# Kernel optimization log

Hardware: AMD Instinct MI355X
Metric: run time of the kernel (lower is better)

## Reference

```python
import jax, jax.numpy as jnp
import numpy as np

B, N, NFEAT = 64, 384, 16
E = 3
NHID, NOUT = 128, 128
ST_HID, ST_OUT = 64, 16


def _xavier(key, shape, fan_in, fan_out):
    a = jnp.sqrt(6.0 / (fan_in + fan_out))
    return jax.random.uniform(key, shape, jnp.float32, -a, a)


def setup_inputs() -> dict:
    key = jax.random.key(0)
    ks = jax.random.split(key, 10)
    x = jax.random.normal(ks[0], (B, N, NFEAT), jnp.float32)
    adj = jax.random.uniform(ks[1], (B, E, N, N), jnp.float32)
    emb_w = _xavier(ks[2], (NFEAT, NFEAT), NFEAT, NFEAT)            # Linear(nfeat,nfeat,bias=False)
    gc1_w = _xavier(ks[3], (E, NFEAT, NHID), NFEAT, NHID)           # (edge_dim,in,out)
    gc2_w = _xavier(ks[4], (E, NHID, NHID), NHID, NHID)             # single middle layer (num_layers-2=1)
    gc3_w = _xavier(ks[5], (E, NHID, NOUT), NHID, NOUT)
    st_w1 = _xavier(ks[6], (ST_HID, NOUT), NOUT, ST_HID)            # nn.Linear stores (out,in)
    st_b1 = jnp.zeros((ST_HID,), jnp.float32)
    st_w2 = jnp.full((2 * ST_OUT, ST_HID), 1e-10, jnp.float32)      # init.constant_(linear2.weight, 1e-10)
    st_b2 = jnp.zeros((2 * ST_OUT,), jnp.float32)
    rescale_w = jnp.zeros((1,), jnp.float32)                        # Rescale weight init zero
    return {"x": x, "adj": adj, "emb_w": emb_w, "gc1_w": gc1_w, "gc2_w": gc2_w,
            "gc3_w": gc3_w, "st_w1": st_w1, "st_b1": st_b1, "st_w2": st_w2,
            "st_b2": st_b2, "rescale_w": rescale_w}


def _rgcn_layer(h, adj, W, relu):
    # support: einsum('bid,edh->beih'), aggregate: einsum('beij,bejh->beih'), then sum over e
    support = jnp.einsum('bnd,edh->benh', h, W)
    out = jnp.einsum('bemn,benh->bemh', adj, support)
    if relu:
        out = jax.nn.relu(out)
    return out.sum(axis=1)  # aggregate='sum' over edge types


def reference(x, adj, emb_w, gc1_w, gc2_w, gc3_w, st_w1, st_b1, st_w2, st_b2, rescale_w):
    h = x @ emb_w.T                                   # emb Linear, no bias
    h = _rgcn_layer(h, adj, gc1_w, True)
    h = _rgcn_layer(h, adj, gc2_w, True)
    h = _rgcn_layer(h, adj, gc3_w, False)             # gc3: use_relu=False
    flat = h.reshape(-1, h.shape[-1])                 # (B*N, nout)
    z = jnp.tanh(flat @ st_w1.T + st_b1) @ st_w2.T + st_b2
    s, t = z[:, :ST_OUT], z[:, ST_OUT:]
    s = jnp.exp(rescale_w) * jnp.tanh(s)              # Rescale(tanh(s))
    return jnp.stack([s, t])                          # (2, B*N, ST_OUT)
```

## Files before the change

kernel.cpp:

```cpp
#include <hip/hip_runtime.h>
#include <math.h>

#define ROWS 24576
#define ADJ_BE (384*384)

typedef _Float16 h4v __attribute__((ext_vector_type(4)));
typedef _Float16 h8v __attribute__((ext_vector_type(8)));
typedef float f32x4 __attribute__((ext_vector_type(4)));

#define SPLIT_SCALE 2048.0f
#define INV_SPLIT_SCALE (1.0f / 2048.0f)

__global__ __launch_bounds__(256) void k_h0split(const float* __restrict__ x,
        const float* __restrict__ emb_w, _Float16* __restrict__ Hh, _Float16* __restrict__ Hl) {
    __shared__ float embL[256];
    int t = threadIdx.x;
    if (t < 64) *(float4*)&embL[4 * t] = *(const float4*)(emb_w + 4 * t);
    __syncthreads();
    int gid = blockIdx.x * 256 + t;
    int b = gid / 384, r = gid % 384;
    const float* xp = x + (size_t)gid * 16;
    float xr[16];
    *(float4*)&xr[0]  = *(const float4*)(xp);
    *(float4*)&xr[4]  = *(const float4*)(xp + 4);
    *(float4*)&xr[8]  = *(const float4*)(xp + 8);
    *(float4*)&xr[12] = *(const float4*)(xp + 12);
    size_t base = (size_t)b * 16 * 384 + r;
#pragma unroll
    for (int d = 0; d < 16; ++d) {
        float acc = 0.f;
#pragma unroll
        for (int k = 0; k < 16; ++k) acc = fmaf(xr[k], embL[d * 16 + k], acc);
        _Float16 h = (_Float16)acc;
        Hh[base + (size_t)d * 384] = h;
        Hl[base + (size_t)d * 384] = (_Float16)((acc - (float)h) * SPLIT_SCALE);
    }
}

__global__ __launch_bounds__(256) void k_adj16(const float* __restrict__ adj,
        const _Float16* __restrict__ Hh, const _Float16* __restrict__ Hl,
        float* __restrict__ T1) {
    int mt = blockIdx.x, e = blockIdx.y, b = blockIdx.z;
    const float* A = adj + (size_t)(b * 3 + e) * ADJ_BE + (size_t)mt * 64 * 384;
    const _Float16* BH = Hh + (size_t)b * 16 * 384;
    const _Float16* BL = Hl + (size_t)b * 16 * 384;

    __shared__ _Float16 Af[2][4][4][17][8];

    int t = threadIdx.x;
    int wave = t >> 6, lane = t & 63;
    int l16 = lane & 15, quad = lane >> 4;
    int r0s = t >> 3, q4s = t & 7;

    f32x4 acc0 = f32x4{0.f, 0.f, 0.f, 0.f};
    f32x4 acc1 = f32x4{0.f, 0.f, 0.f, 0.f};

    float4 ra[2];
    h8v rbh, rbl;
#pragma unroll
    for (int p = 0; p < 2; ++p)
        ra[p] = *(const float4*)(A + (size_t)(r0s + 32 * p) * 384 + 4 * q4s);
    rbh = *(const h8v*)(BH + (size_t)l16 * 384 + 8 * quad);
    rbl = *(const h8v*)(BL + (size_t)l16 * 384 + 8 * quad);

    for (int kc = 0; kc < 12; ++kc) {
#pragma unroll
        for (int p = 0; p < 2; ++p) {
            int r = r0s + 32 * p;
            float vv[4] = {ra[p].x, ra[p].y, ra[p].z, ra[p].w};
            h4v hh, ll;
#pragma unroll
            for (int c = 0; c < 4; ++c) {
                _Float16 h = (_Float16)vv[c];
                hh[c] = h;
                ll[c] = (_Float16)((vv[c] - (float)h) * SPLIT_SCALE);
            }
            *(h4v*)&Af[0][r >> 4][q4s >> 1][r & 15][(q4s & 1) * 4] = hh;
            *(h4v*)&Af[1][r >> 4][q4s >> 1][r & 15][(q4s & 1) * 4] = ll;
        }
        h8v b_h = rbh, b_l = rbl;
        __syncthreads();
        if (kc + 1 < 12) {
            int kn = (kc + 1) * 32;
#pragma unroll
            for (int p = 0; p < 2; ++p)
                ra[p] = *(const float4*)(A + (size_t)(r0s + 32 * p) * 384 + kn + 4 * q4s);
            rbh = *(const h8v*)(BH + (size_t)l16 * 384 + kn + 8 * quad);
            rbl = *(const h8v*)(BL + (size_t)l16 * 384 + kn + 8 * quad);
        }
        h8v a_h = *(const h8v*)&Af[0][wave][quad][l16][0];
        h8v a_l = *(const h8v*)&Af[1][wave][quad][l16][0];
        acc0 = __builtin_amdgcn_mfma_f32_16x16x32_f16(a_h, b_h, acc0, 0, 0, 0);
        acc1 = __builtin_amdgcn_mfma_f32_16x16x32_f16(a_h, b_l, acc1, 0, 0, 0);
        acc1 = __builtin_amdgcn_mfma_f32_16x16x32_f16(a_l, b_h, acc1, 0, 0, 0);
        __syncthreads();
    }
    float* Tp = T1 + ((size_t)(b * 3 + e) * 384 + (size_t)mt * 64 + wave * 16) * 16;
#pragma unroll
    for (int reg = 0; reg < 4; ++reg) {
        float v = fmaf(acc1[reg], INV_SPLIT_SCALE, acc0[reg]);
        Tp[(quad * 4 + reg) * 16 + l16] = v;
    }
}

__global__ __launch_bounds__(256) void k_l1s2(const float* __restrict__ T1,
        const float* __restrict__ W1, float* __restrict__ h1) {
    __shared__ float wL[3][16][128];
    __shared__ float tL[3][64][17];
    int t = threadIdx.x;
    int rt = blockIdx.x;
    int b = rt / 6, m0 = (rt % 6) * 64;
#pragma unroll
    for (int p = 0; p < 6; ++p) {
        int idx = t + p * 256;
        float4 v = *(const float4*)(W1 + (size_t)idx * 4);
        int e = idx / 512, rem = idx % 512;
        int d = rem >> 5, q = rem & 31;
        *(float4*)&wL[e][d][q * 4] = v;
    }
#pragma unroll
    for (int p = 0; p < 3; ++p) {
        int idx = t + p * 256;
        int e = idx >> 8, rem = idx & 255;
        int r = rem >> 2, q = rem & 3;
        float4 v = *(const float4*)(T1 + ((size_t)(b * 3 + e) * 384 + m0 + r) * 16 + q * 4);
        tL[e][r][q*4+0] = v.x; tL[e][r][q*4+1] = v.y; tL[e][r][q*4+2] = v.z; tL[e][r][q*4+3] = v.w;
    }
    __syncthreads();
    int tx = t & 31;
    int ty = t >> 5;
    float tot[8][4] = {};
#pragma unroll
    for (int e = 0; e < 3; ++e) {
        float acc[8][4] = {};
#pragma unroll
        for (int d = 0; d < 16; ++d) {
            float a[8], w[4];
#pragma unroll
            for (int i = 0; i < 8; ++i) a[i] = tL[e][ty + 8 * i][d];
#pragma unroll
            for (int j = 0; j < 4; ++j) w[j] = wL[e][d][tx + 32 * j];
#pragma unroll
            for (int i = 0; i < 8; ++i)
#pragma unroll
                for (int j = 0; j < 4; ++j)
                    acc[i][j] = fmaf(a[i], w[j], acc[i][j]);
        }
#pragma unroll
        for (int i = 0; i < 8; ++i)
#pragma unroll
            for (int j = 0; j < 4; ++j)
                tot[i][j] += fmaxf(acc[i][j], 0.f);
    }
    float* out = h1 + (size_t)rt * 64 * 128;
#pragma unroll
    for (int i = 0; i < 8; ++i)
#pragma unroll
        for (int j = 0; j < 4; ++j)
            out[(ty + 8 * i) * 128 + tx + 32 * j] = tot[i][j];
}

__global__ __launch_bounds__(256) void k_support(const float* __restrict__ hin,
        const float* __restrict__ W, _Float16* __restrict__ Sh, _Float16* __restrict__ Sl) {
    int rt = blockIdx.x, e = blockIdx.y;
    int b = rt / 6, n0 = (rt % 6) * 64;
    const float* Hp = hin + (size_t)rt * 64 * 128;
    const float* Wp = W + (size_t)e * 128 * 128;
    __shared__ float aT[32][68];
    __shared__ float bT[32][132];
    int t = threadIdx.x;
    int tx = t & 15;
    int ty = t >> 4;
    float acc[4][8] = {};
    for (int k0 = 0; k0 < 128; k0 += 32) {
        __syncthreads();
#pragma unroll
        for (int p = 0; p < 2; ++p) {
            int idx = t + p * 256;
            int r = idx >> 3, q = idx & 7;
            float4 v = *(const float4*)(Hp + (size_t)r * 128 + k0 + q * 4);
            aT[q*4+0][r] = v.x; aT[q*4+1][r] = v.y; aT[q*4+2][r] = v.z; aT[q*4+3][r] = v.w;
        }
#pragma unroll
        for (int p = 0; p < 4; ++p) {
            int idx = t + p * 256;
            int r = idx >> 5, q = idx & 31;
            *(float4*)&bT[r][q * 4] = *(const float4*)(Wp + (size_t)(k0 + r) * 128 + q * 4);
        }
        __syncthreads();
#pragma unroll
        for (int k = 0; k < 32; ++k) {
            float4 av = *(const float4*)&aT[k][4 * ty];
            float4 b0 = *(const float4*)&bT[k][4 * tx];
            float4 b1 = *(const float4*)&bT[k][64 + 4 * tx];
            float a[4] = {av.x, av.y, av.z, av.w};
            float bb[8] = {b0.x, b0.y, b0.z, b0.w, b1.x, b1.y, b1.z, b1.w};
#pragma unroll
            for (int i = 0; i < 4; ++i)
#pragma unroll
                for (int j = 0; j < 8; ++j)
                    acc[i][j] = fmaf(a[i], bb[j], acc[i][j]);
        }
    }
    size_t base = (size_t)(b * 3 + e) * 128 * 384;
#pragma unroll
    for (int j = 0; j < 8; ++j) {
        int n = (j < 4) ? (4 * tx + j) : (64 + 4 * tx + j - 4);
        h4v hh, ll;
#pragma unroll
        for (int i = 0; i < 4; ++i) {
            float v = acc[i][j];
            _Float16 h = (_Float16)v;
            hh[i] = h;
            ll[i] = (_Float16)((v - (float)h) * SPLIT_SCALE);
        }
        size_t off = base + (size_t)n * 384 + n0 + 4 * ty;
        *(h4v*)(Sh + off) = hh;
        *(h4v*)(Sl + off) = ll;
    }
}

template <int RELU>
__global__ __launch_bounds__(256, 3) void k_adj_mfma(const float* __restrict__ adj,
        const _Float16* __restrict__ Sh, const _Float16* __restrict__ Sl,
        float* __restrict__ out) {
    int bid = blockIdx.x;
    int xcd = bid & 7, l = bid >> 3;
    int pair = xcd * 24 + (l >> 2);
    int mt = l & 3;
    int b = pair / 3;
    const float* A = adj + (size_t)pair * ADJ_BE + (size_t)mt * 96 * 384;
    const _Float16* Bh = Sh + (size_t)pair * 128 * 384;
    const _Float16* Bl = Sl + (size_t)pair * 128 * 384;
    float* O = out + ((size_t)b * 384 + mt * 96) * 128;

    __shared__ _Float16 Af[2][6][4][17][8];
    __shared__ _Float16 Bf[2][8][4][17][8];

    int t = threadIdx.x;
    int wave = t >> 6, lane = t & 63;
    int l16 = lane & 15, quad = lane >> 4;
    int wm = wave >> 1, wn = wave & 1;
    int r0s = t >> 3, q4s = t & 7;

    f32x4 acc0[3][4], acc1[3][4];
#pragma unroll
    for (int i = 0; i < 3; ++i)
#pragma unroll
        for (int j = 0; j < 4; ++j) {
            acc0[i][j] = f32x4{0.f, 0.f, 0.f, 0.f};
            acc1[i][j] = f32x4{0.f, 0.f, 0.f, 0.f};
        }

    float4 ra[3];
    h8v rb[4];
#pragma unroll
    for (int p = 0; p < 3; ++p)
        ra[p] = *(const float4*)(A + (size_t)(r0s + 32 * p) * 384 + 4 * q4s);
#pragma unroll
    for (int p = 0; p < 4; ++p) {
        int si = t + 256 * (p & 1);
        int n = si >> 2, q8 = si & 3;
        const _Float16* Bsrc = (p < 2) ? Bh : Bl;
        rb[p] = *(const h8v*)(Bsrc + (size_t)n * 384 + 8 * q8);
    }

    for (int k0 = 0; k0 < 384; k0 += 32) {
#pragma unroll
        for (int p = 0; p < 3; ++p) {
            int r = r0s + 32 * p;
            float vv[4] = {ra[p].x, ra[p].y, ra[p].z, ra[p].w};
            h4v hh, ll;
#pragma unroll
            for (int c = 0; c < 4; ++c) {
                _Float16 h = (_Float16)vv[c];
                hh[c] = h;
                ll[c] = (_Float16)((vv[c] - (float)h) * SPLIT_SCALE);
            }
            *(h4v*)&Af[0][r >> 4][q4s >> 1][r & 15][(q4s & 1) * 4] = hh;
            *(h4v*)&Af[1][r >> 4][q4s >> 1][r & 15][(q4s & 1) * 4] = ll;
        }
#pragma unroll
        for (int p = 0; p < 4; ++p) {
            int si = t + 256 * (p & 1);
            int n = si >> 2, q8 = si & 3;
            *(h8v*)&Bf[p >> 1][n >> 4][q8][n & 15][0] = rb[p];
        }
        __syncthreads();
        if (k0 + 32 < 384) {
            int kn = k0 + 32;
#pragma unroll
            for (int p = 0; p < 3; ++p)
                ra[p] = *(const float4*)(A + (size_t)(r0s + 32 * p) * 384 + kn + 4 * q4s);
#pragma unroll
            for (int p = 0; p < 4; ++p) {
                int si = t + 256 * (p & 1);
                int n = si >> 2, q8 = si & 3;
                const _Float16* Bsrc = (p < 2) ? Bh : Bl;
                rb[p] = *(const h8v*)(Bsrc + (size_t)n * 384 + kn + 8 * q8);
            }
        }
        h8v a_h[3], a_l[3];
#pragma unroll
        for (int i = 0; i < 3; ++i) {
            a_h[i] = *(const h8v*)&Af[0][3 * wm + i][quad][l16][0];
            a_l[i] = *(const h8v*)&Af[1][3 * wm + i][quad][l16][0];
        }
#pragma unroll
        for (int j = 0; j < 4; ++j) {
            h8v b_h = *(const h8v*)&Bf[0][4 * wn + j][quad][l16][0];
            h8v b_l = *(const h8v*)&Bf[1][4 * wn + j][quad][l16][0];
#pragma unroll
            for (int i = 0; i < 3; ++i) {
                acc0[i][j] = __builtin_amdgcn_mfma_f32_16x16x32_f16(a_h[i], b_h, acc0[i][j], 0, 0, 0);
                acc1[i][j] = __builtin_amdgcn_mfma_f32_16x16x32_f16(a_h[i], b_l, acc1[i][j], 0, 0, 0);
                acc1[i][j] = __builtin_amdgcn_mfma_f32_16x16x32_f16(a_l[i], b_h, acc1[i][j], 0, 0, 0);
            }
        }
        __syncthreads();
    }
#pragma unroll
    for (int i = 0; i < 3; ++i) {
        int r0 = 48 * wm + 16 * i + quad * 4;
#pragma unroll
        for (int j = 0; j < 4; ++j) {
            int gc = 64 * wn + 16 * j + l16;
#pragma unroll
            for (int reg = 0; reg < 4; ++reg) {
                float v = fmaf(acc1[i][j][reg], INV_SPLIT_SCALE, acc0[i][j][reg]);
                if (RELU) v = fmaxf(v, 0.f);
                atomicAdd(O + (size_t)(r0 + reg) * 128 + gc, v);
            }
        }
    }
}

__global__ void k_zero(float* __restrict__ p, int n4) {
    int i = blockIdx.x * blockDim.x + threadIdx.x;
    if (i < n4) ((float4*)p)[i] = float4{0.f, 0.f, 0.f, 0.f};
}

__global__ __launch_bounds__(256) void k_head(const float* __restrict__ h3,
        const float* __restrict__ st_w1, const float* __restrict__ st_b1,
        const float* __restrict__ st_w2, const float* __restrict__ st_b2,
        const float* __restrict__ rescale_w, float* __restrict__ out) {
    __shared__ float hL[64][132];
    __shared__ float w1L[64][132];
    __shared__ float ytL[64][68];
    __shared__ float w2L[32][68];
    __shared__ float b1L[64], b2L[32];
    int t = threadIdx.x;
    int r0 = blockIdx.x * 64;
#pragma unroll
    for (int p = 0; p < 8; ++p) {
        int idx = t + p * 256;
        int r = idx >> 5, q = idx & 31;
        *(float4*)&hL[r][q * 4] = *(const float4*)(h3 + (size_t)(r0 + r) * 128 + q * 4);
    }
#pragma unroll
    for (int p = 0; p < 8; ++p) {
        int idx = t + p * 256;
        int r = idx >> 5, q = idx & 31;
        *(float4*)&w1L[r][q * 4] = *(const float4*)(st_w1 + (size_t)r * 128 + q * 4);
    }
#pragma unroll
    for (int p = 0; p < 2; ++p) {
        int idx = t + p * 256;
        int r = idx >> 4, q = idx & 15;
        *(float4*)&w2L[r][q * 4] = *(const float4*)(st_w2 + (size_t)r * 64 + q * 4);
    }
    if (t < 64) b1L[t] = st_b1[t];
    else if (t < 96) b2L[t - 64] = st_b2[t - 64];
    __syncthreads();
    int tx = t & 15, ty = t >> 4;
    float acc[4][4] = {};
    for (int d = 0; d < 128; ++d) {
        float a[4], w[4];
#pragma unroll
        for (int i = 0; i < 4; ++i) a[i] = hL[ty + 16 * i][d];
#pragma unroll
        for (int j = 0; j < 4; ++j) w[j] = w1L[tx + 16 * j][d];
#pragma unroll
        for (int i = 0; i < 4; ++i)
#pragma unroll
            for (int j = 0; j < 4; ++j)
                acc[i][j] = fmaf(a[i], w[j], acc[i][j]);
    }
#pragma unroll
    for (int i = 0; i < 4; ++i)
#pragma unroll
        for (int j = 0; j < 4; ++j)
            ytL[ty + 16 * i][tx + 16 * j] = tanhf(acc[i][j] + b1L[tx + 16 * j]);
    __syncthreads();
    int tx8 = t & 7, ty32 = t >> 3;
    float acc2[2][4] = {};
    for (int d = 0; d < 64; ++d) {
        float a[2], w[4];
#pragma unroll
        for (int i = 0; i < 2; ++i) a[i] = ytL[ty32 + 32 * i][d];
#pragma unroll
        for (int j = 0; j < 4; ++j) w[j] = w2L[tx8 + 8 * j][d];
#pragma unroll
        for (int i = 0; i < 2; ++i)
#pragma unroll
            for (int j = 0; j < 4; ++j)
                acc2[i][j] = fmaf(a[i], w[j], acc2[i][j]);
    }
    float er = expf(rescale_w[0]);
#pragma unroll
    for (int i = 0; i < 2; ++i) {
        int r = r0 + ty32 + 32 * i;
#pragma unroll
        for (int j = 0; j < 4; ++j) {
            int c = tx8 + 8 * j;
            float z = acc2[i][j] + b2L[c];
            if (c < 16) out[(size_t)r * 16 + c] = er * tanhf(z);
            else        out[(size_t)(ROWS + r) * 16 + (c - 16)] = z;
        }
    }
}

extern "C" void kernel_launch(void* const* d_in, const int* in_sizes, int n_in,
                              void* d_out, int out_size, void* d_ws, size_t ws_size,
                              hipStream_t stream) {
    const float* x     = (const float*)d_in[0];
    const float* adj   = (const float*)d_in[1];
    const float* emb_w = (const float*)d_in[2];
    const float* gc1   = (const float*)d_in[3];
    const float* gc2   = (const float*)d_in[4];
    const float* gc3   = (const float*)d_in[5];
    const float* st_w1 = (const float*)d_in[6];
    const float* st_b1 = (const float*)d_in[7];
    const float* st_w2 = (const float*)d_in[8];
    const float* st_b2 = (const float*)d_in[9];
    const float* resc  = (const float*)d_in[10];
    float* out = (float*)d_out;
    float* ws  = (float*)d_ws;

    float* T1 = ws;
    float* hA = T1 + 1179648;
    float* hB = hA + 3145728;
    _Float16* Sh = (_Float16*)(hB + 3145728);
    _Float16* Sl = Sh + 9437184;
    _Float16* Hh = (_Float16*)hB;
    _Float16* Hl = Hh + 393216;

    k_h0split<<<96, 256, 0, stream>>>(x, emb_w, Hh, Hl);
    k_adj16<<<dim3(6, 3, 64), 256, 0, stream>>>(adj, Hh, Hl, T1);
    k_l1s2<<<384, 256, 0, stream>>>(T1, gc1, hA);
    k_support<<<dim3(384, 3), 256, 0, stream>>>(hA, gc2, Sh, Sl);
    k_zero<<<3072, 256, 0, stream>>>(hB, 786432);
    k_adj_mfma<1><<<768, 256, 0, stream>>>(adj, Sh, Sl, hB);
    k_support<<<dim3(384, 3), 256, 0, stream>>>(hB, gc3, Sh, Sl);
    k_zero<<<3072, 256, 0, stream>>>(hA, 786432);
    k_adj_mfma<0><<<768, 256, 0, stream>>>(adj, Sh, Sl, hA);
    k_head<<<384, 256, 0, stream>>>(hA, st_w1, st_b1, st_w2, st_b2, resc, out);
}
```

Measured before the change: 434.7 us.

## Fuse edge-type sum into adjacency MFMA kernel, replacing atomics with direct stores

Each block now owns a 48-row tile of one batch and loops over all three edge types in sequence. It applies the ReLU per edge type and accumulates into registers, so it can write its output with plain stores. This removes the zero-fill kernels and the float atomicAdds to global memory. In exchange the grid shrinks from 768 to 512 blocks with smaller per-block M tiles, so each block re-reads the B (support) tiles more per output row. Occupancy is also lowered to 2 blocks per SIMD hint, and half the threads sit idle during A tile loads.

```diff
diff --git a/kernel.cpp b/kernel.cpp
--- a/kernel.cpp
+++ b/kernel.cpp
@@ -221,61 +221,69 @@
 }
 
 template <int RELU>
-__global__ __launch_bounds__(256, 3) void k_adj_mfma(const float* __restrict__ adj,
+__global__ __launch_bounds__(256, 2) void k_adj_fused(const float* __restrict__ adj,
         const _Float16* __restrict__ Sh, const _Float16* __restrict__ Sl,
         float* __restrict__ out) {
     int bid = blockIdx.x;
     int xcd = bid & 7, l = bid >> 3;
-    int pair = xcd * 24 + (l >> 2);
-    int mt = l & 3;
-    int b = pair / 3;
-    const float* A = adj + (size_t)pair * ADJ_BE + (size_t)mt * 96 * 384;
-    const _Float16* Bh = Sh + (size_t)pair * 128 * 384;
-    const _Float16* Bl = Sl + (size_t)pair * 128 * 384;
-    float* O = out + ((size_t)b * 384 + mt * 96) * 128;
-
-    __shared__ _Float16 Af[2][6][4][17][8];
+    int b = xcd * 8 + (l >> 3);
+    int mt = l & 7;
+    const float* A0 = adj + (size_t)(b * 3) * ADJ_BE + (size_t)mt * 48 * 384;
+    const _Float16* Bh0 = Sh + (size_t)(b * 3) * 128 * 384;
+    const _Float16* Bl0 = Sl + (size_t)(b * 3) * 128 * 384;
+    float* O = out + ((size_t)b * 384 + mt * 48) * 128;
+
+    __shared__ _Float16 Af[2][3][4][17][8];
     __shared__ _Float16 Bf[2][8][4][17][8];
 
     int t = threadIdx.x;
     int wave = t >> 6, lane = t & 63;
     int l16 = lane & 15, quad = lane >> 4;
-    int wm = wave >> 1, wn = wave & 1;
     int r0s = t >> 3, q4s = t & 7;
 
-    f32x4 acc0[3][4], acc1[3][4];
+    f32x4 acc0[3][2], acc1[3][2], tot[3][2];
 #pragma unroll
     for (int i = 0; i < 3; ++i)
 #pragma unroll
-        for (int j = 0; j < 4; ++j) {
+        for (int j = 0; j < 2; ++j) {
             acc0[i][j] = f32x4{0.f, 0.f, 0.f, 0.f};
             acc1[i][j] = f32x4{0.f, 0.f, 0.f, 0.f};
-        }
-
-    float4 ra[3];
+            tot[i][j]  = f32x4{0.f, 0.f, 0.f, 0.f};
+        }
+
+    float4 ra[2];
     h8v rb[4];
-#pragma unroll
-    for (int p = 0; p < 3; ++p)
-        ra[p] = *(const float4*)(A + (size_t)(r0s + 32 * p) * 384 + 4 * q4s);
+
+    const float* Ap = A0;
+    const _Float16* Bhp = Bh0;
+    const _Float16* Blp = Bl0;
+    int kn = 0;
+
+#pragma unroll
+    for (int p = 0; p < 2; ++p)
+        if (p == 0 || t < 128)
+            ra[p] = *(const float4*)(Ap + (size_t)(r0s + 32 * p) * 384 + kn + 4 * q4s);
 #pragma unroll
     for (int p = 0; p < 4; ++p) {
         int si = t + 256 * (p & 1);
         int n = si >> 2, q8 = si & 3;
-        const _Float16* Bsrc = (p < 2) ? Bh : Bl;
-        rb[p] = *(const h8v*)(Bsrc + (size_t)n * 384 + 8 * q8);
-    }
-
-    for (int k0 = 0; k0 < 384; k0 += 32) {
-#pragma unroll
-        for (int p = 0; p < 3; ++p) {
+        const _Float16* Bsrc = (p < 2) ? Bhp : Blp;
+        rb[p] = *(const h8v*)(Bsrc + (size_t)n * 384 + kn + 8 * q8);
+    }
+    kn += 32;
+
+    for (int c = 0; c < 36; ++c) {
+#pragma unroll
+        for (int p = 0; p < 2; ++p) {
+            if (p == 1 && t >= 128) break;
             int r = r0s + 32 * p;
             float vv[4] = {ra[p].x, ra[p].y, ra[p].z, ra[p].w};
             h4v hh, ll;
 #pragma unroll
-            for (int c = 0; c < 4; ++c) {
-                _Float16 h = (_Float16)vv[c];
-                hh[c] = h;
-                ll[c] = (_Float16)((vv[c] - (float)h) * SPLIT_SCALE);
+            for (int cc = 0; cc < 4; ++cc) {
+                _Float16 h = (_Float16)vv[cc];
+                hh[cc] = h;
+                ll[cc] = (_Float16)((vv[cc] - (float)h) * SPLIT_SCALE);
             }
             *(h4v*)&Af[0][r >> 4][q4s >> 1][r & 15][(q4s & 1) * 4] = hh;
             *(h4v*)&Af[1][r >> 4][q4s >> 1][r & 15][(q4s & 1) * 4] = ll;
@@ -287,29 +295,36 @@
             *(h8v*)&Bf[p >> 1][n >> 4][q8][n & 15][0] = rb[p];
         }
         __syncthreads();
-        if (k0 + 32 < 384) {
-            int kn = k0 + 32;
-#pragma unroll
-            for (int p = 0; p < 3; ++p)
-                ra[p] = *(const float4*)(A + (size_t)(r0s + 32 * p) * 384 + kn + 4 * q4s);
+        if (c + 1 < 36) {
+            if (kn == 384) {
+                kn = 0;
+                Ap += (size_t)ADJ_BE;
+                Bhp += (size_t)128 * 384;
+                Blp += (size_t)128 * 384;
+            }
+#pragma unroll
+            for (int p = 0; p < 2; ++p)
+                if (p == 0 || t < 128)
+                    ra[p] = *(const float4*)(Ap + (size_t)(r0s + 32 * p) * 384 + kn + 4 * q4s);
 #pragma unroll
             for (int p = 0; p < 4; ++p) {
                 int si = t + 256 * (p & 1);
                 int n = si >> 2, q8 = si & 3;
-                const _Float16* Bsrc = (p < 2) ? Bh : Bl;
+                const _Float16* Bsrc = (p < 2) ? Bhp : Blp;
                 rb[p] = *(const h8v*)(Bsrc + (size_t)n * 384 + kn + 8 * q8);
             }
+            kn += 32;
         }
         h8v a_h[3], a_l[3];
 #pragma unroll
         for (int i = 0; i < 3; ++i) {
-            a_h[i] = *(const h8v*)&Af[0][3 * wm + i][quad][l16][0];
-            a_l[i] = *(const h8v*)&Af[1][3 * wm + i][quad][l16][0];
-        }
-#pragma unroll
-        for (int j = 0; j < 4; ++j) {
-            h8v b_h = *(const h8v*)&Bf[0][4 * wn + j][quad][l16][0];
-            h8v b_l = *(const h8v*)&Bf[1][4 * wn + j][quad][l16][0];
+            a_h[i] = *(const h8v*)&Af[0][i][quad][l16][0];
+            a_l[i] = *(const h8v*)&Af[1][i][quad][l16][0];
+        }
+#pragma unroll
+        for (int j = 0; j < 2; ++j) {
+            h8v b_h = *(const h8v*)&Bf[0][2 * wave + j][quad][l16][0];
+            h8v b_l = *(const h8v*)&Bf[1][2 * wave + j][quad][l16][0];
 #pragma unroll
             for (int i = 0; i < 3; ++i) {
                 acc0[i][j] = __builtin_amdgcn_mfma_f32_16x16x32_f16(a_h[i], b_h, acc0[i][j], 0, 0, 0);
@@ -317,27 +332,34 @@
                 acc1[i][j] = __builtin_amdgcn_mfma_f32_16x16x32_f16(a_l[i], b_h, acc1[i][j], 0, 0, 0);
             }
         }
+        if (c % 12 == 11) {
+#pragma unroll
+            for (int i = 0; i < 3; ++i)
+#pragma unroll
+                for (int j = 0; j < 2; ++j) {
+#pragma unroll
+                    for (int reg = 0; reg < 4; ++reg) {
+                        float v = fmaf(acc1[i][j][reg], INV_SPLIT_SCALE, acc0[i][j][reg]);
+                        if (RELU) v = fmaxf(v, 0.f);
+                        tot[i][j][reg] += v;
+                    }
+                    acc0[i][j] = f32x4{0.f, 0.f, 0.f, 0.f};
+                    acc1[i][j] = f32x4{0.f, 0.f, 0.f, 0.f};
+                }
+        }
         __syncthreads();
     }
 #pragma unroll
     for (int i = 0; i < 3; ++i) {
-        int r0 = 48 * wm + 16 * i + quad * 4;
-#pragma unroll
-        for (int j = 0; j < 4; ++j) {
-            int gc = 64 * wn + 16 * j + l16;
-#pragma unroll
-            for (int reg = 0; reg < 4; ++reg) {
-                float v = fmaf(acc1[i][j][reg], INV_SPLIT_SCALE, acc0[i][j][reg]);
-                if (RELU) v = fmaxf(v, 0.f);
-                atomicAdd(O + (size_t)(r0 + reg) * 128 + gc, v);
-            }
-        }
-    }
-}
-
-__global__ void k_zero(float* __restrict__ p, int n4) {
-    int i = blockIdx.x * blockDim.x + threadIdx.x;
-    if (i < n4) ((float4*)p)[i] = float4{0.f, 0.f, 0.f, 0.f};
+        int r0 = 16 * i + quad * 4;
+#pragma unroll
+        for (int j = 0; j < 2; ++j) {
+            int gc = 32 * wave + 16 * j + l16;
+#pragma unroll
+            for (int reg = 0; reg < 4; ++reg)
+                O[(size_t)(r0 + reg) * 128 + gc] = tot[i][j][reg];
+        }
+    }
 }
 
 __global__ __launch_bounds__(256) void k_head(const float* __restrict__ h3,
@@ -449,10 +471,8 @@
     k_adj16<<<dim3(6, 3, 64), 256, 0, stream>>>(adj, Hh, Hl, T1);
     k_l1s2<<<384, 256, 0, stream>>>(T1, gc1, hA);
     k_support<<<dim3(384, 3), 256, 0, stream>>>(hA, gc2, Sh, Sl);
-    k_zero<<<3072, 256, 0, stream>>>(hB, 786432);
-    k_adj_mfma<1><<<768, 256, 0, stream>>>(adj, Sh, Sl, hB);
+    k_adj_fused<1><<<512, 256, 0, stream>>>(adj, Sh, Sl, hB);
     k_support<<<dim3(384, 3), 256, 0, stream>>>(hB, gc3, Sh, Sl);
-    k_zero<<<3072, 256, 0, stream>>>(hA, 786432);
-    k_adj_mfma<0><<<768, 256, 0, stream>>>(adj, Sh, Sl, hA);
+    k_adj_fused<0><<<512, 256, 0, stream>>>(adj, Sh, Sl, hA);
     k_head<<<384, 256, 0, stream>>>(hA, st_w1, st_b1, st_w2, st_b2, resc, out);
 }
```

After: 374.8 us (median of 2 runs). 1.16x faster.
